# Kernel optimization log

Hardware: AMD Instinct MI355X
Metric: run time of the kernel (lower is better)

The kernel has to match this reference:

```python
import jax, jax.numpy as jnp
import numpy as np

B, C, T, H, K = 512, 64, 512, 128, 16
EPS_BN = 1e-5


def setup_inputs() -> dict:
    key = jax.random.key(0)
    ks = jax.random.split(key, 8)
    s = 0.05
    return {
        "x": jax.random.normal(ks[0], (B, C, T), jnp.float32),
        "conv1_w": jax.random.normal(ks[1], (H, C, 3), jnp.float32) * s,
        "conv1_b": jnp.zeros((H,), jnp.float32),
        "conv2_w": jax.random.normal(ks[2], (H, H, 3), jnp.float32) * s,
        "conv2_b": jnp.zeros((H,), jnp.float32),
        "bnt1_g": jnp.ones((H,), jnp.float32), "bnt1_b": jnp.zeros((H,), jnp.float32),
        "bnt2_g": jnp.ones((H,), jnp.float32), "bnt2_b": jnp.zeros((H,), jnp.float32),
        "W1": jax.random.normal(ks[3], (T, H), jnp.float32) * s, "b1": jnp.zeros((H,), jnp.float32),
        "g1": jnp.ones((H,), jnp.float32), "be1": jnp.zeros((H,), jnp.float32),
        "W2": jax.random.normal(ks[4], (H, H), jnp.float32) * s, "b2": jnp.zeros((H,), jnp.float32),
        "g2": jnp.ones((H,), jnp.float32), "be2": jnp.zeros((H,), jnp.float32),
        "W3": jax.random.normal(ks[5], (H, H), jnp.float32) * s, "b3": jnp.zeros((H,), jnp.float32),
        "g3": jnp.ones((H,), jnp.float32), "be3": jnp.zeros((H,), jnp.float32),
    }


def _bn_nc(z, g, b):
    # BatchNorm1d on (N, C) with batch statistics (training-mode normalization)
    m = z.mean(0)
    v = z.var(0)
    return (z - m) * jax.lax.rsqrt(v + EPS_BN) * g + b


def _bn_ncl(z, g, b):
    # BatchNorm1d on (N, C, L)
    m = z.mean((0, 2), keepdims=True)
    v = z.var((0, 2), keepdims=True)
    return (z - m) * jax.lax.rsqrt(v + EPS_BN) * g[None, :, None] + b[None, :, None]


def _conv1d(z, w, b):
    y = jax.lax.conv_general_dilated(z, w, (1,), "SAME",
                                     dimension_numbers=("NCH", "OIH", "NCH"))
    return y + b[None, :, None]


def _forward(x, conv1_w, conv1_b, conv2_w, conv2_b, bnt1_g, bnt1_b, bnt2_g, bnt2_b,
             W1, b1, g1, be1, W2, b2, g2, be2, W3, b3, g3, be3):
    # temporal branch: computed but unused in the output (faithful to the source)
    ht = jax.nn.relu(_bn_ncl(_conv1d(x, conv1_w, conv1_b), bnt1_g, bnt1_b))
    ht = jax.nn.relu(_bn_ncl(_conv1d(ht, conv2_w, conv2_b), bnt2_g, bnt2_b))

    # dynamic graph: cosine similarity averaged over batch, top-k neighbors per channel
    xn = x / jnp.maximum(jnp.linalg.norm(x, axis=2, keepdims=True), 1e-12)
    sim = jnp.einsum("bct,bdt->cd", xn, xn) / x.shape[0]  # (C, C)
    _, nbr = jax.lax.top_k(sim, K)                        # (C, K)
    src = jnp.repeat(jnp.arange(C), K)                    # (C*K,)
    dst = nbr.reshape(-1)                                 # (C*K,)
    offs = (jnp.arange(B) * C)[:, None]
    N = B * C
    sl = jnp.arange(N)
    # edge_index[0]=source node i, edge_index[1]=its top-k neighbor; plus GCN self-loops
    es = jnp.concatenate([(src[None, :] + offs).reshape(-1), sl])
    ed = jnp.concatenate([(dst[None, :] + offs).reshape(-1), sl])

    deg = jax.ops.segment_sum(jnp.ones(es.shape[0], x.dtype), ed, num_segments=N)
    dinv = jax.lax.rsqrt(deg)  # deg >= 1 due to self-loops
    enorm = dinv[es] * dinv[ed]

    def gcn(h, W, b):
        hw = h @ W
        return jax.ops.segment_sum(hw[es] * enorm[:, None], ed, num_segments=N) + b

    # source does permute(0,2,1).view(B*C, T): a flat reshape of the (B, T, C) tensor
    nodes = jnp.transpose(x, (0, 2, 1)).reshape(N, T)
    h = jax.nn.relu(_bn_nc(gcn(nodes, W1, b1), g1, be1))
    h = jax.nn.relu(_bn_nc(gcn(h, W2, b2), g2, be2))
    h = jax.nn.relu(_bn_nc(gcn(h, W3, b3), g3, be3))
    return h.reshape(B, C * H)


def reference(x, conv1_w, conv1_b, conv2_w, conv2_b, bnt1_g, bnt1_b, bnt2_g, bnt2_b,
              W1, b1, g1, be1, W2, b2, g2, be2, W3, b3, g3, be3):
    return _forward(x, conv1_w, conv1_b, conv2_w, conv2_b, bnt1_g, bnt1_b,
                    bnt2_g, bnt2_b, W1, b1, g1, be1, W2, b2, g2, be2,
                    W3, b3, g3, be3)
```

## Files before the change

### kernel.cpp

```cpp
#include <hip/hip_runtime.h>
#include <math.h>

#define B_  512
#define C_  64
#define T_  512
#define H_  128
#define N_  (B_*C_)

typedef unsigned int   uint_;
typedef unsigned short ushort_;
typedef unsigned long long ull_;

typedef __attribute__((ext_vector_type(8))) short bf8v;
typedef __attribute__((ext_vector_type(4))) float f4v;

#define OFF_SIMP   0u
#define OFF_Z2     0u
#define OFF_Z1     8388608u
#define OFF_Z3     16777216u
#define OFF_WT1    25165824u
#define OFF_WT2    25296896u
#define OFF_WT3    25329664u
#define OFF_MASKS  25362432u
#define OFF_BNPART 25406464u
#define OFF_BNP2   25930752u

__device__ __forceinline__ ushort_ f2bf(float f) {
    uint_ u = __float_as_uint(f);
    u = (u + 0x7FFFu + ((u >> 16) & 1u)) >> 16;
    return (ushort_)u;
}
__device__ __forceinline__ float bf2f(ushort_ s) {
    return __uint_as_float(((uint_)s) << 16);
}

__device__ __forceinline__ void m_preamble_wave0(const ull_* __restrict__ masks,
                                                 ull_* nbrmS, float* dvS, int t)
{
    if (t < 64) {
        ull_ mask = masks[t];
        nbrmS[t] = mask;
        int deg = 1;
#pragma unroll
        for (int d = 0; d < 64; ++d) {
            ull_ bal = __ballot((int)((mask >> d) & 1ull));
            if (t == d) deg += (int)__popcll(bal);
        }
        dvS[t] = 1.0f / sqrtf((float)deg);
    }
}

__device__ __forceinline__ void m_build(const ull_* nbrmS, const float* dvS,
                                        int t, uint_ m8[8])
{
    const int d = t >> 2, q = t & 3;
    const float dvd = dvS[d];
#pragma unroll
    for (int p = 0; p < 8; ++p) {
        int c0 = 16 * q + 2 * p, c1 = c0 + 1;
        float w0 = (float)((int)((nbrmS[c0] >> d) & 1ull) + (c0 == d ? 1 : 0));
        float w1 = (float)((int)((nbrmS[c1] >> d) & 1ull) + (c1 == d ? 1 : 0));
        m8[p] = (uint_)f2bf(w0 * dvS[c0] * dvd) |
                ((uint_)f2bf(w1 * dvS[c1] * dvd) << 16);
    }
}

__global__ __launch_bounds__(256) void k_gramw(const float* __restrict__ x,
    float* __restrict__ simpart,
    const float* __restrict__ W1, const float* __restrict__ W2,
    const float* __restrict__ W3,
    ushort_* __restrict__ Wt1, ushort_* __restrict__ Wt2, ushort_* __restrict__ Wt3)
{
    __shared__ __align__(16) char smem[35584];
    __shared__ float  gd[64];
    __shared__ double rn[64];
    const int blk = blockIdx.x;
    const int t = threadIdx.x;

    if (blk < 512) {
        ushort_* Xh = (ushort_*)smem;
        ushort_* Xl = (ushort_*)(smem + 17408);
        const int b = blk;
        const int w = t >> 6, l = t & 63;
        const int lr = l & 15, lg = l >> 4;
        const int r0 = (w >> 1) * 2, c0 = (w & 1) * 2;

        f4v acc[2][2];
#pragma unroll
        for (int i = 0; i < 2; ++i)
#pragma unroll
            for (int j = 0; j < 2; ++j) acc[i][j] = (f4v)0.f;

        const float* xb = x + (size_t)b * (C_ * T_);

        for (int j = 0; j < 4; ++j) {
#pragma unroll
            for (int it = 0; it < 8; ++it) {
                int i = t + 256 * it;
                int c = i >> 5, t4 = i & 31;
                float4 v = *(const float4*)&xb[(size_t)c * T_ + 128 * j + 4 * t4];
                ushort_ h0 = f2bf(v.x), h1 = f2bf(v.y), h2 = f2bf(v.z), h3 = f2bf(v.w);
                uint2 ph;
                ph.x = (uint_)h0 | ((uint_)h1 << 16);
                ph.y = (uint_)h2 | ((uint_)h3 << 16);
                float e0 = v.x - bf2f(h0), e1 = v.y - bf2f(h1);
                float e2 = v.z - bf2f(h2), e3 = v.w - bf2f(h3);
                uint2 pl;
                pl.x = (uint_)f2bf(e0) | ((uint_)f2bf(e1) << 16);
                pl.y = (uint_)f2bf(e2) | ((uint_)f2bf(e3) << 16);
                *(uint2*)&Xh[c * 136 + 4 * t4] = ph;
                *(uint2*)&Xl[c * 136 + 4 * t4] = pl;
            }
            __syncthreads();

#pragma unroll
            for (int s = 0; s < 4; ++s) {
                bf8v ah[2], al[2], bh[2], bl[2];
#pragma unroll
                for (int i = 0; i < 2; ++i) {
                    ah[i] = *(const bf8v*)&Xh[(16 * (r0 + i) + lr) * 136 + 32 * s + 8 * lg];
                    al[i] = *(const bf8v*)&Xl[(16 * (r0 + i) + lr) * 136 + 32 * s + 8 * lg];
                    bh[i] = *(const bf8v*)&Xh[(16 * (c0 + i) + lr) * 136 + 32 * s + 8 * lg];
                    bl[i] = *(const bf8v*)&Xl[(16 * (c0 + i) + lr) * 136 + 32 * s + 8 * lg];
                }
#pragma unroll
                for (int i = 0; i < 2; ++i)
#pragma unroll
                    for (int jj = 0; jj < 2; ++jj) {
                        acc[i][jj] = __builtin_amdgcn_mfma_f32_16x16x32_bf16(ah[i], bh[jj], acc[i][jj], 0, 0, 0);
                        acc[i][jj] = __builtin_amdgcn_mfma_f32_16x16x32_bf16(ah[i], bl[jj], acc[i][jj], 0, 0, 0);
                        acc[i][jj] = __builtin_amdgcn_mfma_f32_16x16x32_bf16(al[i], bh[jj], acc[i][jj], 0, 0, 0);
                    }
            }
            __syncthreads();
        }

        if (r0 == c0) {
#pragma unroll
            for (int d = 0; d < 2; ++d)
                if (lg == (lr >> 2)) gd[16 * (r0 + d) + lr] = acc[d][d][lr & 3];
        }
        __syncthreads();
        if (t < 64) rn[t] = 1.0 / fmax(sqrt((double)gd[t]), 1e-12);
        __syncthreads();

        float* sp = simpart + (size_t)b * 4096;
#pragma unroll
        for (int i = 0; i < 2; ++i)
#pragma unroll
            for (int jj = 0; jj < 2; ++jj)
#pragma unroll
                for (int reg = 0; reg < 4; ++reg) {
                    int rc = 16 * (r0 + i) + 4 * lg + reg;
                    int cc = 16 * (c0 + jj) + lr;
                    sp[rc * 64 + cc] = (float)((double)acc[i][jj][reg] * rn[rc] * rn[cc]);
                }
    } else {
        float* L = (float*)smem;
        const int pblk = blk - 512;
        if (pblk < 8) {
            for (int it = 0; it < 8; ++it) {
                int i = t + 256 * it;
                int ri = i >> 5, f4 = i & 31;
                int m = ri >> 3, cr = ri & 7;
                *(float4*)&L[ri * 132 + 4 * f4] =
                    *(const float4*)&W1[(size_t)(64 * m + 8 * pblk + cr) * H_ + 4 * f4];
            }
            __syncthreads();
            int f = t >> 1, half = t & 1;
            uint_ buf[16];
#pragma unroll
            for (int jj = 0; jj < 16; ++jj) {
                int k0 = 32 * half + 2 * jj;
                int c0 = k0 >> 3, m0 = k0 & 7;
                int c1 = (k0 + 1) >> 3, m1 = (k0 + 1) & 7;
                buf[jj] = (uint_)f2bf(L[(m0 * 8 + c0) * 132 + f]) |
                          ((uint_)f2bf(L[(m1 * 8 + c1) * 132 + f]) << 16);
            }
            ushort_* dst = Wt1 + (size_t)f * 512 + 64 * pblk + 32 * half;
#pragma unroll
            for (int q = 0; q < 4; ++q) {
                uint4 vv = {buf[4 * q], buf[4 * q + 1], buf[4 * q + 2], buf[4 * q + 3]};
                *(uint4*)&dst[8 * q] = vv;
            }
        } else {
            const float* W = (pblk < 10) ? W2 : W3;
            ushort_*     O = (pblk < 10) ? Wt2 : Wt3;
            int kb = (pblk - 8) & 1;
            for (int it = 0; it < 8; ++it) {
                int i = t + 256 * it;
                int ri = i >> 5, f4 = i & 31;
                *(float4*)&L[ri * 132 + 4 * f4] =
                    *(const float4*)&W[(size_t)(64 * kb + ri) * H_ + 4 * f4];
            }
            __syncthreads();
            int f = t >> 1, half = t & 1;
            uint_ buf[16];
#pragma unroll
            for (int jj = 0; jj < 16; ++jj) {
                int k0 = 32 * half + 2 * jj;
                buf[jj] = (uint_)f2bf(L[k0 * 132 + f]) |
                          ((uint_)f2bf(L[(k0 + 1) * 132 + f]) << 16);
            }
            ushort_* dst = O + (size_t)f * 128 + 64 * kb + 32 * half;
#pragma unroll
            for (int q = 0; q < 4; ++q) {
                uint4 vv = {buf[4 * q], buf[4 * q + 1], buf[4 * q + 2], buf[4 * q + 3]};
                *(uint4*)&dst[8 * q] = vv;
            }
        }
    }
}

__global__ __launch_bounds__(256) void k_simrank(const float* __restrict__ simpart,
                                                 ull_* __restrict__ masks)
{
    __shared__ double part[4][64];
    __shared__ double sd[64];
    const int c = blockIdx.x;
    const int t = threadIdx.x;
    const int d = t & 63, g = t >> 6;

    double a = 0.0;
    const float* sp = simpart + (size_t)c * 64 + d;
    for (int i = 0; i < 128; ++i)
        a += (double)sp[(size_t)(g + 4 * i) * 4096];
    part[g][d] = a;
    __syncthreads();

    if (t < 64) {
        double s = ((part[0][t] + part[1][t]) + part[2][t]) + part[3][t];
        sd[t] = s;
        int rank = 0;
#pragma unroll
        for (int dp = 0; dp < 64; ++dp) {
            double w = sd[dp];
            rank += (w > s || (w == s && dp < t)) ? 1 : 0;
        }
        ull_ m = __ballot(rank < 16);
        if (t == 0) masks[c] = m;
    }
}

__device__ __forceinline__ void mfma_epilogue(char* smem, int b, int t,
    f4v acc[8], const float* __restrict__ bias, const uint_ m8[8],
    ushort_* __restrict__ Zout, float* __restrict__ bnpart)
{
    const int l = t & 63, w = t >> 6;
    const int lr = l & 15, lg = l >> 4;

    ushort_* Yt  = (ushort_*)smem;
    ushort_* Ml  = (ushort_*)(smem + 22528);
    ushort_* Zst = (ushort_*)(smem + 33792);

#pragma unroll
    for (int nt = 0; nt < 8; ++nt) {
        uint2 p;
        p.x = (uint_)f2bf(acc[nt][0]) | ((uint_)f2bf(acc[nt][1]) << 16);
        p.y = (uint_)f2bf(acc[nt][2]) | ((uint_)f2bf(acc[nt][3]) << 16);
        *(uint2*)&Yt[(16 * nt + lr) * 88 + 16 * w + 4 * lg] = p;
    }
    {
        const int d = t >> 2, q = t & 3;
        uint4 v0 = {m8[0], m8[1], m8[2], m8[3]};
        uint4 v1 = {m8[4], m8[5], m8[6], m8[7]};
        *(uint4*)&Ml[d * 88 + 16 * q]     = v0;
        *(uint4*)&Ml[d * 88 + 16 * q + 8] = v1;
    }
    __syncthreads();

    f4v z[8];
#pragma unroll
    for (int nt = 0; nt < 8; ++nt) z[nt] = (f4v)0.f;
#pragma unroll
    for (int cs = 0; cs < 2; ++cs) {
        bf8v mf = *(const bf8v*)&Ml[(16 * w + lr) * 88 + 32 * cs + 8 * lg];
#pragma unroll
        for (int nt = 0; nt < 8; ++nt) {
            bf8v yf = *(const bf8v*)&Yt[(16 * nt + lr) * 88 + 32 * cs + 8 * lg];
            z[nt] = __builtin_amdgcn_mfma_f32_16x16x32_bf16(mf, yf, z[nt], 0, 0, 0);
        }
    }

#pragma unroll
    for (int nt = 0; nt < 8; ++nt) {
        float bv = bias[16 * nt + lr];
#pragma unroll
        for (int reg = 0; reg < 4; ++reg)
            Zst[(16 * w + 4 * lg + reg) * 136 + 16 * nt + lr] = f2bf(z[nt][reg] + bv);
    }
    __syncthreads();

    if (t < 128) {
        float s = 0.f, s2 = 0.f;
        for (int r = 0; r < 64; ++r) {
            float v = bf2f(Zst[r * 136 + t]);
            s += v; s2 += v * v;
        }
        bnpart[b * 256 + t]       = s;
        bnpart[b * 256 + 128 + t] = s2;
    }
#pragma unroll
    for (int it = 0; it < 4; ++it) {
        int i = t + 256 * it;
        int r = i >> 4, seg = i & 15;
        *(uint4*)&Zout[((size_t)(b * 64 + r)) * 128 + 8 * seg] =
            *(const uint4*)&Zst[r * 136 + 8 * seg];
    }
}

__global__ __launch_bounds__(256) void k_mgemm1(const float* __restrict__ x,
    const ushort_* __restrict__ Wt, const float* __restrict__ bias,
    const ull_* __restrict__ masks, ushort_* __restrict__ Zout,
    float* __restrict__ bnpart)
{
    __shared__ __align__(16) char smem[51456];
    __shared__ ull_  nbrmS[64];
    __shared__ float dvS[64];
    ushort_* Al = (ushort_*)smem;
    ushort_* Wl = (ushort_*)(smem + 16640);

    const int b = blockIdx.x;
    const int t = threadIdx.x;
    const int l = t & 63, w = t >> 6;
    const int lr = l & 15, lg = l >> 4;

    m_preamble_wave0(masks, nbrmS, dvS, t);

    f4v acc[8];
#pragma unroll
    for (int nt = 0; nt < 8; ++nt) acc[nt] = (f4v)0.f;

    const float* xb = x + (size_t)b * (C_ * T_);

    for (int j = 0; j < 4; ++j) {
#pragma unroll
        for (int it = 0; it < 8; ++it) {
            int i = t + 256 * it;
            int cr = i >> 7, t4 = i & 127;
            float4 v = *(const float4*)&xb[(size_t)(16 * j + cr) * T_ + 4 * t4];
            uint2 p;
            p.x = (uint_)f2bf(v.x) | ((uint_)f2bf(v.y) << 16);
            p.y = (uint_)f2bf(v.z) | ((uint_)f2bf(v.w) << 16);
            *(uint2*)&Al[cr * 520 + 4 * t4] = p;
        }
#pragma unroll
        for (int it = 0; it < 8; ++it) {
            int i = t + 256 * it;
            int f = i >> 4, seg = i & 15;
            *(uint4*)&Wl[f * 136 + 8 * seg] =
                *(const uint4*)&Wt[(size_t)f * 512 + 128 * j + 8 * seg];
        }
        __syncthreads();
#pragma unroll
        for (int s = 0; s < 4; ++s) {
            bf8v af = *(const bf8v*)&Al[(4 * s + lg) * 520 + 128 * w + 8 * lr];
#pragma unroll
            for (int nt = 0; nt < 8; ++nt) {
                bf8v bfv = *(const bf8v*)&Wl[(16 * nt + lr) * 136 + 32 * s + 8 * lg];
                acc[nt] = __builtin_amdgcn_mfma_f32_16x16x32_bf16(af, bfv, acc[nt], 0, 0, 0);
            }
        }
        __syncthreads();
    }

    uint_ m8[8];
    m_build(nbrmS, dvS, t, m8);
    mfma_epilogue(smem, b, t, acc, bias, m8, Zout, bnpart);
}

__global__ __launch_bounds__(256) void k_mgemm23(const ushort_* __restrict__ Zin,
    const double* __restrict__ bnp2, const float* __restrict__ g,
    const float* __restrict__ be, const ushort_* __restrict__ Wt,
    const float* __restrict__ bias, const ull_* __restrict__ masks,
    ushort_* __restrict__ Zout, float* __restrict__ bnpart)
{
    __shared__ __align__(16) char smem[52224];
    __shared__ float ssL[256];
    __shared__ ull_  nbrmS[64];
    __shared__ float dvS[64];
    ushort_* Al = (ushort_*)smem;
    ushort_* Wl = (ushort_*)(smem + 17408);

    const int b = blockIdx.x;
    const int t = threadIdx.x;
    const int l = t & 63, w = t >> 6;
    const int lr = l & 15, lg = l >> 4;

    {
        double* sumsL = (double*)smem;
        double a = 0.0;
        for (int q = 0; q < 32; ++q) a += bnp2[(size_t)q * 256 + t];
        sumsL[t] = a;
        m_preamble_wave0(masks, nbrmS, dvS, t);
        __syncthreads();
        if (t < 128) {
            double s = sumsL[t], s2 = sumsL[128 + t];
            double mean = s * (1.0 / 32768.0);
            double var  = s2 * (1.0 / 32768.0) - mean * mean;
            double rstd = 1.0 / sqrt(var + 1e-5);
            float sc = (float)((double)g[t] * rstd);
            ssL[t]       = sc;
            ssL[128 + t] = (float)((double)be[t] - mean * (double)sc);
        }
        __syncthreads();
    }

    f4v acc[8];
#pragma unroll
    for (int nt = 0; nt < 8; ++nt) acc[nt] = (f4v)0.f;

#pragma unroll
    for (int it = 0; it < 4; ++it) {
        int i = t + 256 * it;
        int r = i >> 4, seg = i & 15;
        uint4 v = *(const uint4*)&Zin[((size_t)(b * 64 + r)) * 128 + 8 * seg];
        uint_ w0[4] = {v.x, v.y, v.z, v.w};
        uint_ o[4];
#pragma unroll
        for (int p = 0; p < 4; ++p) {
            int f0 = 8 * seg + 2 * p;
            float z0 = bf2f((ushort_)(w0[p] & 0xFFFF));
            float z1 = bf2f((ushort_)(w0[p] >> 16));
            float h0 = fmaxf(fmaf(z0, ssL[f0],     ssL[128 + f0]),     0.f);
            float h1 = fmaxf(fmaf(z1, ssL[f0 + 1], ssL[128 + f0 + 1]), 0.f);
            o[p] = (uint_)f2bf(h0) | ((uint_)f2bf(h1) << 16);
        }
        uint4 ov = {o[0], o[1], o[2], o[3]};
        *(uint4*)&Al[r * 136 + 8 * seg] = ov;
    }
#pragma unroll
    for (int it = 0; it < 8; ++it) {
        int i = t + 256 * it;
        int f = i >> 4, seg = i & 15;
        *(uint4*)&Wl[f * 136 + 8 * seg] =
            *(const uint4*)&Wt[(size_t)f * 128 + 8 * seg];
    }
    __syncthreads();
#pragma unroll
    for (int s = 0; s < 4; ++s) {
        bf8v af = *(const bf8v*)&Al[(16 * w + lr) * 136 + 32 * s + 8 * lg];
#pragma unroll
        for (int nt = 0; nt < 8; ++nt) {
            bf8v bfv = *(const bf8v*)&Wl[(16 * nt + lr) * 136 + 32 * s + 8 * lg];
            acc[nt] = __builtin_amdgcn_mfma_f32_16x16x32_bf16(af, bfv, acc[nt], 0, 0, 0);
        }
    }
    __syncthreads();

    uint_ m8[8];
    m_build(nbrmS, dvS, t, m8);
    mfma_epilogue(smem, b, t, acc, bias, m8, Zout, bnpart);
}

__global__ __launch_bounds__(256) void k_bnA(const float* __restrict__ bnpart,
                                             double* __restrict__ bnp2)
{
    const int t = threadIdx.x, g = blockIdx.x;
    double a = 0.0;
    for (int i = 0; i < 16; ++i)
        a += (double)bnpart[(size_t)(16 * g + i) * 256 + t];
    bnp2[(size_t)g * 256 + t] = a;
}

__global__ __launch_bounds__(256) void k_out(const ushort_* __restrict__ Z,
    const double* __restrict__ bnp2, const float* __restrict__ g,
    const float* __restrict__ be, float* __restrict__ out)
{
    __shared__ double sumsL[256];
    __shared__ float  ssL[256];
    const int b = blockIdx.x;
    const int t = threadIdx.x;

    double a = 0.0;
    for (int q = 0; q < 32; ++q) a += bnp2[(size_t)q * 256 + t];
    sumsL[t] = a;
    __syncthreads();
    if (t < 128) {
        double s = sumsL[t], s2 = sumsL[128 + t];
        double mean = s * (1.0 / 32768.0);
        double var  = s2 * (1.0 / 32768.0) - mean * mean;
        double rstd = 1.0 / sqrt(var + 1e-5);
        float sc = (float)((double)g[t] * rstd);
        ssL[t]       = sc;
        ssL[128 + t] = (float)((double)be[t] - mean * (double)sc);
    }
    __syncthreads();

    const size_t base = (size_t)b * 64 * 128;
#pragma unroll
    for (int it = 0; it < 8; ++it) {
        int i = t + 256 * it;
        int r = i >> 5, s = i & 31;
        uint2 v = *(const uint2*)&Z[base + (size_t)r * 128 + 4 * s];
        float4 sc = *(const float4*)&ssL[4 * s];
        float4 sh = *(const float4*)&ssL[128 + 4 * s];
        float z0 = bf2f((ushort_)(v.x & 0xFFFF));
        float z1 = bf2f((ushort_)(v.x >> 16));
        float z2 = bf2f((ushort_)(v.y & 0xFFFF));
        float z3 = bf2f((ushort_)(v.y >> 16));
        float4 o;
        o.x = fmaxf(fmaf(z0, sc.x, sh.x), 0.f);
        o.y = fmaxf(fmaf(z1, sc.y, sh.y), 0.f);
        o.z = fmaxf(fmaf(z2, sc.z, sh.z), 0.f);
        o.w = fmaxf(fmaf(z3, sc.w, sh.w), 0.f);
        *(float4*)&out[base + (size_t)r * 128 + 4 * s] = o;
    }
}

extern "C" void kernel_launch(void* const* d_in, const int* in_sizes, int n_in,
                              void* d_out, int out_size, void* d_ws, size_t ws_size,
                              hipStream_t stream)
{
    (void)in_sizes; (void)n_in; (void)out_size; (void)ws_size;

    const float* x   = (const float*)d_in[0];
    const float* W1  = (const float*)d_in[9];
    const float* b1  = (const float*)d_in[10];
    const float* g1  = (const float*)d_in[11];
    const float* be1 = (const float*)d_in[12];
    const float* W2  = (const float*)d_in[13];
    const float* b2  = (const float*)d_in[14];
    const float* g2  = (const float*)d_in[15];
    const float* be2 = (const float*)d_in[16];
    const float* W3  = (const float*)d_in[17];
    const float* b3  = (const float*)d_in[18];
    const float* g3  = (const float*)d_in[19];
    const float* be3 = (const float*)d_in[20];

    char* ws = (char*)d_ws;
    float*   simp   = (float*)(ws + OFF_SIMP);
    ull_*    masks  = (ull_*)(ws + OFF_MASKS);
    ushort_* Wt1    = (ushort_*)(ws + OFF_WT1);
    ushort_* Wt2    = (ushort_*)(ws + OFF_WT2);
    ushort_* Wt3    = (ushort_*)(ws + OFF_WT3);
    float*   bnpart = (float*)(ws + OFF_BNPART);
    double*  bnp2   = (double*)(ws + OFF_BNP2);
    ushort_* Z1     = (ushort_*)(ws + OFF_Z1);
    ushort_* Z2     = (ushort_*)(ws + OFF_Z2);
    ushort_* Z3     = (ushort_*)(ws + OFF_Z3);
    float*   out    = (float*)d_out;

    k_gramw<<<dim3(524), dim3(256), 0, stream>>>(x, simp, W1, W2, W3, Wt1, Wt2, Wt3);
    k_simrank<<<dim3(64), dim3(256), 0, stream>>>(simp, masks);

    k_mgemm1<<<dim3(512), dim3(256), 0, stream>>>(x, Wt1, b1, masks, Z1, bnpart);
    k_bnA<<<dim3(32), dim3(256), 0, stream>>>(bnpart, bnp2);

    k_mgemm23<<<dim3(512), dim3(256), 0, stream>>>(Z1, bnp2, g1, be1, Wt2, b2, masks, Z2, bnpart);
    k_bnA<<<dim3(32), dim3(256), 0, stream>>>(bnpart, bnp2);

    k_mgemm23<<<dim3(512), dim3(256), 0, stream>>>(Z2, bnp2, g2, be2, Wt3, b3, masks, Z3, bnpart);
    k_bnA<<<dim3(32), dim3(256), 0, stream>>>(bnpart, bnp2);

    k_out<<<dim3(512), dim3(256), 0, stream>>>(Z3, bnp2, g3, be3, out);
}
```

Before: 99.92 us.

## Cache bf16 x from gram kernel and stream GEMM operands via global_load_lds

The gram kernel now also writes the bf16-rounded x to a workspace buffer. The first GCN GEMM reads that half-size copy instead of re-reading and converting fp32 x, and loads both it and the weight tiles directly into LDS with global_load_lds, dropping the row padding. The GEMM2/3 kernel also moves its weight loads to global_load_lds and issues them earlier, and the similarity reduction runs with 1024 threads per block. The trade is extra global writes in the gram kernel and unpadded LDS rows, which may cause bank conflicts.

Measured after the change: 99.02 us. About the same (-0.9%).

```diff
diff --git a/kernel.cpp b/kernel.cpp
--- a/kernel.cpp
+++ b/kernel.cpp
@@ -24,6 +24,7 @@
 #define OFF_MASKS  25362432u
 #define OFF_BNPART 25406464u
 #define OFF_BNP2   25930752u
+#define OFF_XH     33554432u
 
 __device__ __forceinline__ ushort_ f2bf(float f) {
     uint_ u = __float_as_uint(f);
@@ -32,6 +33,12 @@
 }
 __device__ __forceinline__ float bf2f(ushort_ s) {
     return __uint_as_float(((uint_)s) << 16);
+}
+
+__device__ __forceinline__ void gload_lds16(const void* g, void* l) {
+    __builtin_amdgcn_global_load_lds(
+        (const __attribute__((address_space(1))) void*)g,
+        (__attribute__((address_space(3))) void*)l, 16, 0, 0);
 }
 
 __device__ __forceinline__ void m_preamble_wave0(const ull_* __restrict__ masks,
@@ -66,7 +73,7 @@
 }
 
 __global__ __launch_bounds__(256) void k_gramw(const float* __restrict__ x,
-    float* __restrict__ simpart,
+    float* __restrict__ simpart, ushort_* __restrict__ Xhg,
     const float* __restrict__ W1, const float* __restrict__ W2,
     const float* __restrict__ W3,
     ushort_* __restrict__ Wt1, ushort_* __restrict__ Wt2, ushort_* __restrict__ Wt3)
@@ -110,6 +117,7 @@
                 pl.y = (uint_)f2bf(e2) | ((uint_)f2bf(e3) << 16);
                 *(uint2*)&Xh[c * 136 + 4 * t4] = ph;
                 *(uint2*)&Xl[c * 136 + 4 * t4] = pl;
+                *(uint2*)&Xhg[(((size_t)(b * 64 + c)) << 9) + 128 * j + 4 * t4] = ph;
             }
             __syncthreads();
 
@@ -212,10 +220,10 @@
     }
 }
 
-__global__ __launch_bounds__(256) void k_simrank(const float* __restrict__ simpart,
-                                                 ull_* __restrict__ masks)
-{
-    __shared__ double part[4][64];
+__global__ __launch_bounds__(1024) void k_simrank(const float* __restrict__ simpart,
+                                                  ull_* __restrict__ masks)
+{
+    __shared__ double part[16][64];
     __shared__ double sd[64];
     const int c = blockIdx.x;
     const int t = threadIdx.x;
@@ -223,13 +231,15 @@
 
     double a = 0.0;
     const float* sp = simpart + (size_t)c * 64 + d;
-    for (int i = 0; i < 128; ++i)
-        a += (double)sp[(size_t)(g + 4 * i) * 4096];
+    for (int i = 0; i < 32; ++i)
+        a += (double)sp[(size_t)(g + 16 * i) * 4096];
     part[g][d] = a;
     __syncthreads();
 
     if (t < 64) {
-        double s = ((part[0][t] + part[1][t]) + part[2][t]) + part[3][t];
+        double s = 0.0;
+#pragma unroll
+        for (int q = 0; q < 16; ++q) s += part[q][t];
         sd[t] = s;
         int rank = 0;
 #pragma unroll
@@ -309,7 +319,7 @@
     }
 }
 
-__global__ __launch_bounds__(256) void k_mgemm1(const float* __restrict__ x,
+__global__ __launch_bounds__(256) void k_mgemm1(const ushort_* __restrict__ Xh,
     const ushort_* __restrict__ Wt, const float* __restrict__ bias,
     const ull_* __restrict__ masks, ushort_* __restrict__ Zout,
     float* __restrict__ bnpart)
@@ -318,7 +328,7 @@
     __shared__ ull_  nbrmS[64];
     __shared__ float dvS[64];
     ushort_* Al = (ushort_*)smem;
-    ushort_* Wl = (ushort_*)(smem + 16640);
+    ushort_* Wl = (ushort_*)(smem + 16384);
 
     const int b = blockIdx.x;
     const int t = threadIdx.x;
@@ -331,33 +341,29 @@
 #pragma unroll
     for (int nt = 0; nt < 8; ++nt) acc[nt] = (f4v)0.f;
 
-    const float* xb = x + (size_t)b * (C_ * T_);
-
     for (int j = 0; j < 4; ++j) {
-#pragma unroll
-        for (int it = 0; it < 8; ++it) {
-            int i = t + 256 * it;
-            int cr = i >> 7, t4 = i & 127;
-            float4 v = *(const float4*)&xb[(size_t)(16 * j + cr) * T_ + 4 * t4];
-            uint2 p;
-            p.x = (uint_)f2bf(v.x) | ((uint_)f2bf(v.y) << 16);
-            p.y = (uint_)f2bf(v.z) | ((uint_)f2bf(v.w) << 16);
-            *(uint2*)&Al[cr * 520 + 4 * t4] = p;
-        }
-#pragma unroll
-        for (int it = 0; it < 8; ++it) {
-            int i = t + 256 * it;
-            int f = i >> 4, seg = i & 15;
-            *(uint4*)&Wl[f * 136 + 8 * seg] =
-                *(const uint4*)&Wt[(size_t)f * 512 + 128 * j + 8 * seg];
+        {
+            const char* asrc = (const char*)(Xh + (((size_t)(b * 64 + 16 * j)) << 9)) + t * 16;
+            char* adst = smem + t * 16;
+#pragma unroll
+            for (int i2 = 0; i2 < 4; ++i2)
+                gload_lds16(asrc + i2 * 4096, adst + i2 * 4096);
+        }
+        {
+            const int fr = t >> 4, seg = t & 15;
+            const char* wsrc = (const char*)(Wt + (size_t)fr * 512 + 128 * j + seg * 8);
+            char* wdst = smem + 16384 + t * 16;
+#pragma unroll
+            for (int i2 = 0; i2 < 8; ++i2)
+                gload_lds16(wsrc + i2 * 16384, wdst + i2 * 4096);
         }
         __syncthreads();
 #pragma unroll
         for (int s = 0; s < 4; ++s) {
-            bf8v af = *(const bf8v*)&Al[(4 * s + lg) * 520 + 128 * w + 8 * lr];
+            bf8v af = *(const bf8v*)&Al[(4 * s + lg) * 512 + 128 * w + 8 * lr];
 #pragma unroll
             for (int nt = 0; nt < 8; ++nt) {
-                bf8v bfv = *(const bf8v*)&Wl[(16 * nt + lr) * 136 + 32 * s + 8 * lg];
+                bf8v bfv = *(const bf8v*)&Wl[(16 * nt + lr) * 128 + 32 * s + 8 * lg];
                 acc[nt] = __builtin_amdgcn_mfma_f32_16x16x32_bf16(af, bfv, acc[nt], 0, 0, 0);
             }
         }
@@ -406,6 +412,14 @@
         __syncthreads();
     }
 
+    {
+        const char* wsrc = (const char*)Wt + t * 16;
+        char* wdst = smem + 17408 + t * 16;
+#pragma unroll
+        for (int i2 = 0; i2 < 8; ++i2)
+            gload_lds16(wsrc + i2 * 4096, wdst + i2 * 4096);
+    }
+
     f4v acc[8];
 #pragma unroll
     for (int nt = 0; nt < 8; ++nt) acc[nt] = (f4v)0.f;
@@ -429,20 +443,13 @@
         uint4 ov = {o[0], o[1], o[2], o[3]};
         *(uint4*)&Al[r * 136 + 8 * seg] = ov;
     }
-#pragma unroll
-    for (int it = 0; it < 8; ++it) {
-        int i = t + 256 * it;
-        int f = i >> 4, seg = i & 15;
-        *(uint4*)&Wl[f * 136 + 8 * seg] =
-            *(const uint4*)&Wt[(size_t)f * 128 + 8 * seg];
-    }
     __syncthreads();
 #pragma unroll
     for (int s = 0; s < 4; ++s) {
         bf8v af = *(const bf8v*)&Al[(16 * w + lr) * 136 + 32 * s + 8 * lg];
 #pragma unroll
         for (int nt = 0; nt < 8; ++nt) {
-            bf8v bfv = *(const bf8v*)&Wl[(16 * nt + lr) * 136 + 32 * s + 8 * lg];
+            bf8v bfv = *(const bf8v*)&Wl[(16 * nt + lr) * 128 + 32 * s + 8 * lg];
             acc[nt] = __builtin_amdgcn_mfma_f32_16x16x32_bf16(af, bfv, acc[nt], 0, 0, 0);
         }
     }
@@ -536,15 +543,16 @@
     ushort_* Wt3    = (ushort_*)(ws + OFF_WT3);
     float*   bnpart = (float*)(ws + OFF_BNPART);
     double*  bnp2   = (double*)(ws + OFF_BNP2);
+    ushort_* Xh     = (ushort_*)(ws + OFF_XH);
     ushort_* Z1     = (ushort_*)(ws + OFF_Z1);
     ushort_* Z2     = (ushort_*)(ws + OFF_Z2);
     ushort_* Z3     = (ushort_*)(ws + OFF_Z3);
     float*   out    = (float*)d_out;
 
-    k_gramw<<<dim3(524), dim3(256), 0, stream>>>(x, simp, W1, W2, W3, Wt1, Wt2, Wt3);
-    k_simrank<<<dim3(64), dim3(256), 0, stream>>>(simp, masks);
-
-    k_mgemm1<<<dim3(512), dim3(256), 0, stream>>>(x, Wt1, b1, masks, Z1, bnpart);
+    k_gramw<<<dim3(524), dim3(256), 0, stream>>>(x, simp, Xh, W1, W2, W3, Wt1, Wt2, Wt3);
+    k_simrank<<<dim3(64), dim3(1024), 0, stream>>>(simp, masks);
+
+    k_mgemm1<<<dim3(512), dim3(256), 0, stream>>>(Xh, Wt1, b1, masks, Z1, bnpart);
     k_bnA<<<dim3(32), dim3(256), 0, stream>>>(bnpart, bnp2);
 
     k_mgemm23<<<dim3(512), dim3(256), 0, stream>>>(Z1, bnp2, g1, be1, Wt2, b2, masks, Z2, bnpart);
```
